# Kernel optimization log

Hardware: AMD Instinct MI355X
Metric: run time of the kernel (lower is better)

## Reference

```python
import jax, jax.numpy as jnp
import numpy as np
import itertools

DIM_X, DIM_Y = 3, 3
MAX_DIGIT = DIM_X * DIM_Y          # 9
NUM_NODES = MAX_DIGIT ** 2         # 81
EMBED = 16
HID = 96
BATCH = 256
ITERS = 4


def determine_edges(dim_x, dim_y):
    md = dim_x * dim_y
    rows = []
    for r in range(md):
        for c in range(md):
            s = {(r, i) for i in range(md)} | {(i, c) for i in range(md)}
            xm, ym = r // dim_x * dim_x, c // dim_y * dim_y
            s |= set(itertools.product(range(xm, xm + dim_x), range(ym, ym + dim_y)))
            s -= {(r, c)}
            rows.append(sorted(i * md + j for i, j in s))
    return np.asarray(rows, dtype=np.int32)  # [81, 20]


def mlp3(x, w0, b0, w1, b1, w2, b2):
    # MLP([a,b,c,d]): two ReLU hidden layers, linear output
    x = jax.nn.relu(x @ w0.T + b0)
    x = jax.nn.relu(x @ w1.T + b1)
    return x @ w2.T + b2


def setup_inputs() -> dict:
    key = jax.random.key(0)
    keys = iter(jax.random.split(key, 40))

    def lin(din, dout):
        kw, kb = jax.random.split(next(keys))
        lim = 1.0 / np.sqrt(din)
        w = jax.random.uniform(kw, (dout, din), jnp.float32, -lim, lim)
        b = jax.random.uniform(kb, (dout,), jnp.float32, -lim, lim)
        return w, b

    embed = jax.random.normal(next(keys), (MAX_DIGIT + 1, EMBED), jnp.float32)

    in_w0, in_b0 = lin(EMBED, HID); in_w1, in_b1 = lin(HID, HID); in_w2, in_b2 = lin(HID, HID)
    f_w0, f_b0 = lin(2 * HID, HID); f_w1, f_b1 = lin(HID, HID); f_w2, f_b2 = lin(HID, HID)
    g_w0, g_b0 = lin(2 * HID, HID); g_w1, g_b1 = lin(HID, HID); g_w2, g_b2 = lin(HID, HID)
    r_w0, r_b0 = lin(HID, HID); r_w1, r_b1 = lin(HID, HID); r_w2, r_b2 = lin(HID, MAX_DIGIT)

    lim = 1.0 / np.sqrt(HID)
    lstm_wih = jax.random.uniform(next(keys), (4 * HID, HID), jnp.float32, -lim, lim)
    lstm_whh = jax.random.uniform(next(keys), (4 * HID, HID), jnp.float32, -lim, lim)
    lstm_bih = jax.random.uniform(next(keys), (4 * HID,), jnp.float32, -lim, lim)
    lstm_bhh = jax.random.uniform(next(keys), (4 * HID,), jnp.float32, -lim, lim)

    grids = jax.random.randint(next(keys), (BATCH, NUM_NODES), 0, MAX_DIGIT + 1)
    c0 = jax.random.normal(next(keys), (BATCH * NUM_NODES, HID), jnp.float32)
    edges = jnp.asarray(determine_edges(DIM_X, DIM_Y))

    return dict(embed=embed,
                in_w0=in_w0, in_b0=in_b0, in_w1=in_w1, in_b1=in_b1, in_w2=in_w2, in_b2=in_b2,
                f_w0=f_w0, f_b0=f_b0, f_w1=f_w1, f_b1=f_b1, f_w2=f_w2, f_b2=f_b2,
                g_w0=g_w0, g_b0=g_b0, g_w1=g_w1, g_b1=g_b1, g_w2=g_w2, g_b2=g_b2,
                lstm_wih=lstm_wih, lstm_whh=lstm_whh, lstm_bih=lstm_bih, lstm_bhh=lstm_bhh,
                r_w0=r_w0, r_b0=r_b0, r_w1=r_w1, r_b1=r_b1, r_w2=r_w2, r_b2=r_b2,
                c0=c0, grids=grids, edges=edges, iters=ITERS)


def reference(embed,
              in_w0, in_b0, in_w1, in_b1, in_w2, in_b2,
              f_w0, f_b0, f_w1, f_b1, f_w2, f_b2,
              g_w0, g_b0, g_w1, g_b1, g_w2, g_b2,
              lstm_wih, lstm_whh, lstm_bih, lstm_bhh,
              r_w0, r_b0, r_w1, r_b1, r_w2, r_b2,
              c0, grids, edges, iters):
    B, N = grids.shape
    K = edges.shape[1]
    emb = embed[grids]                                   # [B, N, EMBED]
    X = mlp3(emb, in_w0, in_b0, in_w1, in_b1, in_w2, in_b2)  # [B, N, HID]
    H = X
    h = X.reshape(B * N, HID)
    c = c0
    outputs = []
    for _ in range(iters):
        # gather neighbor states: [B, N, K, HID]
        Hn = H[:, edges]
        Hs = jnp.broadcast_to(H[:, :, None, :], Hn.shape)
        pair = jnp.concatenate([Hs, Hn], axis=-1)        # [B, N, K, 2*HID]
        M = mlp3(pair, f_w0, f_b0, f_w1, f_b1, f_w2, f_b2).sum(axis=2)  # [B, N, HID]
        gin = mlp3(jnp.concatenate([X, M], axis=-1),
                   g_w0, g_b0, g_w1, g_b1, g_w2, g_b2).reshape(B * N, HID)
        # single-step LSTM (torch gate order: i, f, g, o)
        gates = gin @ lstm_wih.T + lstm_bih + h @ lstm_whh.T + lstm_bhh
        gi, gf, gg, go = jnp.split(gates, 4, axis=-1)
        c = jax.nn.sigmoid(gf) * c + jax.nn.sigmoid(gi) * jnp.tanh(gg)
        h = jax.nn.sigmoid(go) * jnp.tanh(c)
        H = h.reshape(B, N, HID)
        outputs.append(mlp3(H, r_w0, r_b0, r_w1, r_b1, r_w2, r_b2))  # [B, N, MAX_DIGIT]
    return jnp.stack(outputs)  # [iters, B, N, MAX_DIGIT]
```

## Files before the change

### kernel.cpp

```cpp
#include <hip/hip_runtime.h>
#include <hip/hip_bf16.h>

typedef __hip_bfloat16 bf16;
typedef __attribute__((ext_vector_type(8))) short short8;
typedef __attribute__((ext_vector_type(8))) __bf16 bf16x8;
typedef __attribute__((ext_vector_type(4))) float f32x4;

#define BN 20736
#define NNODE 81
#define KNB 20

__device__ inline float bf2f(short s) {
  union { unsigned u; float f; } x; x.u = ((unsigned)(unsigned short)s) << 16; return x.f;
}
__device__ inline short f2bf(float f) {
  __hip_bfloat16 h = __float2bfloat16(f);
  return *reinterpret_cast<short*>(&h);
}
__device__ inline bf16x8 ld8(const bf16* p) {
  return __builtin_bit_cast(bf16x8, *(const short8*)p);
}

__device__ inline void zacc3(f32x4 acc[3]) {
  #pragma unroll
  for (int nt = 0; nt < 3; ++nt) acc[nt] = (f32x4){0.f, 0.f, 0.f, 0.f};
}
__device__ inline void load_w48(const bf16* __restrict__ W, int ldw, int n0, int lr, int lq,
                                bf16x8 wf[3][3]) {
  #pragma unroll
  for (int nt = 0; nt < 3; ++nt)
    #pragma unroll
    for (int ks = 0; ks < 3; ++ks)
      wf[nt][ks] = ld8(&W[(size_t)(n0 + nt * 16 + lr) * ldw + ks * 32 + lq * 8]);
}
__device__ inline void gemm48(const bf16x8 af[3], const bf16x8 wf[3][3], f32x4 acc[3]) {
  #pragma unroll
  for (int ks = 0; ks < 3; ++ks)
    #pragma unroll
    for (int nt = 0; nt < 3; ++nt)
      acc[nt] = __builtin_amdgcn_mfma_f32_16x16x32_bf16(af[ks], wf[nt][ks], acc[nt], 0, 0, 0);
}
__device__ inline void acc_store_cs(float* xw, const f32x4 acc[3], int lr, int lq, int n0) {
  #pragma unroll
  for (int nt = 0; nt < 3; ++nt)
    #pragma unroll
    for (int r = 0; r < 4; ++r)
      xw[(lq * 4 + r) * 100 + n0 + nt * 16 + lr] = acc[nt][r];
}
__device__ inline void xbuf_frag(const float* xw, int lr, int lq,
                                 const float* __restrict__ bias, float bscale,
                                 const bf16* __restrict__ residRow, int act,
                                 bf16x8 af[3]) {
  #pragma unroll
  for (int ks = 0; ks < 3; ++ks) {
    const int c0 = ks * 32 + lq * 8;
    float4 x0 = *(const float4*)&xw[lr * 100 + c0];
    float4 x1 = *(const float4*)&xw[lr * 100 + c0 + 4];
    float xv[8] = {x0.x, x0.y, x0.z, x0.w, x1.x, x1.y, x1.z, x1.w};
    if (bias) {
      float4 b0 = *(const float4*)&bias[c0];
      float4 b1 = *(const float4*)&bias[c0 + 4];
      float bv[8] = {b0.x, b0.y, b0.z, b0.w, b1.x, b1.y, b1.z, b1.w};
      #pragma unroll
      for (int j = 0; j < 8; ++j) xv[j] += bscale * bv[j];
    }
    if (residRow) {
      short8 r8 = *(const short8*)&residRow[c0];
      #pragma unroll
      for (int j = 0; j < 8; ++j) xv[j] += bf2f(r8[j]);
    }
    short8 o;
    #pragma unroll
    for (int j = 0; j < 8; ++j) {
      float v = xv[j];
      if (act) v = fmaxf(v, 0.f);
      o[j] = f2bf(v);
    }
    af[ks] = __builtin_bit_cast(bf16x8, o);
  }
}
__device__ inline void store_frag(bf16* dst, int lq, const bf16x8 af[3]) {
  #pragma unroll
  for (int ks = 0; ks < 3; ++ks)
    *(short8*)&dst[ks * 32 + lq * 8] = __builtin_bit_cast(short8, af[ks]);
}

__global__ __launch_bounds__(256) void prep_k(
    const float* in_w1, const float* in_w2, const float* f_w1, const float* f_w2,
    const float* g_w1, const float* g_w2, const float* r_w0, const float* r_w1,
    const float* r_w2, const float* wih, const float* whh, const float* g_w0,
    const float* f_w0, const float* in_w0, const float* f_b0,
    bf16* inw1b, bf16* inw2b, bf16* fw1b, bf16* fw2b,
    bf16* gw1b, bf16* gw2b, bf16* rw0b, bf16* rw1b,
    bf16* rw2b, bf16* wihb, bf16* whhb, bf16* gw0b,
    bf16* wfnb, bf16* w0pb, float* bias_fn)
{
  int idx = blockIdx.x * 256 + threadIdx.x;
  int y = blockIdx.y;
  const float* src = nullptr; bf16* dst = nullptr; int cnt = 0;
  switch (y) {
    case 0:  src = in_w1; dst = inw1b; cnt = 9216;  break;
    case 1:  src = in_w2; dst = inw2b; cnt = 9216;  break;
    case 2:  src = f_w1;  dst = fw1b;  cnt = 9216;  break;
    case 3:  src = f_w2;  dst = fw2b;  cnt = 9216;  break;
    case 4:  src = g_w1;  dst = gw1b;  cnt = 9216;  break;
    case 5:  src = g_w2;  dst = gw2b;  cnt = 9216;  break;
    case 6:  src = r_w0;  dst = rw0b;  cnt = 9216;  break;
    case 7:  src = r_w1;  dst = rw1b;  cnt = 9216;  break;
    case 8:  src = r_w2;  dst = rw2b;  cnt = 864;   break;
    case 9:  src = wih;   dst = wihb;  cnt = 36864; break;
    case 10: src = whh;   dst = whhb;  cnt = 36864; break;
    case 11: src = g_w0;  dst = gw0b;  cnt = 18432; break;
    case 12: {
      if (idx < 18432) {
        int n = idx / 96, k = idx - n * 96;
        float v = (n < 96) ? f_w0[n * 192 + k] : f_w0[(n - 96) * 192 + 96 + k];
        wfnb[idx] = __float2bfloat16(v);
      }
      return;
    }
    case 13: {
      if (idx < 3072) {
        int n = idx >> 5, k = idx & 31;
        w0pb[idx] = __float2bfloat16(k < 16 ? in_w0[n * 16 + k] : 0.f);
      }
      return;
    }
    default: {
      if (idx < 192) bias_fn[idx] = (idx < 96) ? f_b0[idx] : 0.f;
      return;
    }
  }
  if (idx < cnt) dst[idx] = __float2bfloat16(src[idx]);
}

__global__ __launch_bounds__(256) void embed_k(const float* __restrict__ embed,
                                               const int* __restrict__ grids,
                                               bf16* __restrict__ emb) {
  int idx = blockIdx.x * 256 + threadIdx.x;
  if (idx >= BN * 32) return;
  int r = idx >> 5, k = idx & 31;
  emb[idx] = __float2bfloat16(k < 16 ? embed[grids[r] * 16 + k] : 0.f);
}

__global__ __launch_bounds__(256) void fused_in_k(
    const bf16* __restrict__ emb, const bf16* __restrict__ w0pb, const float* __restrict__ in_b0,
    const bf16* __restrict__ inw1b, const float* __restrict__ in_b1,
    const bf16* __restrict__ inw2b, const float* __restrict__ in_b2,
    const bf16* __restrict__ gw0b, const float* __restrict__ g_b0,
    const bf16* __restrict__ wfnb, const float* __restrict__ bias_fn,
    bf16* __restrict__ X, bf16* __restrict__ Xg, bf16* __restrict__ P)
{
  __shared__ float xbuf[2][2][1600];
  const int t = threadIdx.x, w = t >> 6, lane = t & 63, lr = lane & 15, lq = lane >> 4;
  const int mh = w >> 1, ch = w & 1, n0 = ch * 48;
  const int m0 = blockIdx.x * 32 + mh * 16;
  float* x0 = xbuf[0][mh];
  float* x1 = xbuf[1][mh];
  bf16x8 wf[3][3]; f32x4 acc[3]; bf16x8 af[3];

  bf16x8 a0 = ld8(&emb[(size_t)(m0 + lr) * 32 + lq * 8]);
  #pragma unroll
  for (int nt = 0; nt < 3; ++nt)
    wf[nt][0] = ld8(&w0pb[(size_t)(n0 + nt * 16 + lr) * 32 + lq * 8]);
  zacc3(acc);
  #pragma unroll
  for (int nt = 0; nt < 3; ++nt)
    acc[nt] = __builtin_amdgcn_mfma_f32_16x16x32_bf16(a0, wf[nt][0], acc[nt], 0, 0, 0);
  acc_store_cs(x0, acc, lr, lq, n0);
  __syncthreads();
  xbuf_frag(x0, lr, lq, in_b0, 1.f, nullptr, 1, af);
  load_w48(inw1b, 96, n0, lr, lq, wf); zacc3(acc); gemm48(af, wf, acc);
  acc_store_cs(x1, acc, lr, lq, n0);
  __syncthreads();
  xbuf_frag(x1, lr, lq, in_b1, 1.f, nullptr, 1, af);
  load_w48(inw2b, 96, n0, lr, lq, wf); zacc3(acc); gemm48(af, wf, acc);
  acc_store_cs(x0, acc, lr, lq, n0);
  __syncthreads();
  bf16x8 xf[3];
  xbuf_frag(x0, lr, lq, in_b2, 1.f, nullptr, 0, xf);
  if (ch == 0) store_frag(&X[(size_t)(m0 + lr) * 96], lq, xf);
  load_w48(gw0b, 192, n0, lr, lq, wf); zacc3(acc); gemm48(xf, wf, acc);
  acc_store_cs(x1, acc, lr, lq, n0);
  __syncthreads();
  xbuf_frag(x1, lr, lq, g_b0, 1.f, nullptr, 0, af);
  if (ch == 0) store_frag(&Xg[(size_t)(m0 + lr) * 96], lq, af);
  #pragma unroll
  for (int ph = 0; ph < 2; ++ph) {
    float* xb = ph ? x1 : x0;
    load_w48(wfnb + (size_t)ph * 96 * 96, 96, n0, lr, lq, wf); zacc3(acc); gemm48(xf, wf, acc);
    acc_store_cs(xb, acc, lr, lq, n0);
    __syncthreads();
    xbuf_frag(xb, lr, lq, bias_fn + ph * 96, 1.f, nullptr, 0, af);
    if (ch == 0) store_frag(&P[(size_t)(m0 + lr) * 192 + ph * 96], lq, af);
  }
}

__global__ __launch_bounds__(256) void edge_k(
    const bf16* __restrict__ P, const bf16* __restrict__ w1bf,
    const float* __restrict__ b1, const int* __restrict__ edges,
    const bf16* __restrict__ fw2b, const float* __restrict__ f_b2,
    bf16* __restrict__ M)
{
  __shared__ short zs[160 * 104];
  __shared__ short sbuf[16 * 104];
  const int t = threadIdx.x;
  const int ng0 = blockIdx.x * 2;
  for (int i = t; i < 8 * 104; i += 256) sbuf[(8 + i / 104) * 104 + (i % 104)] = 0;
  for (int cc = t; cc < 160 * 12; cc += 256) {
    int zrow = cc / 12, c8 = cc - zrow * 12;
    int g = zrow >= 80 ? 1 : 0;
    int row = zrow - g * 80;
    int p = row / 20, j = row - p * 20;
    int gr = (ng0 + g) * 4 + p;
    int b = gr / NNODE, i = gr - b * NNODE;
    int e = edges[i * KNB + j];
    short8 a8 = *(const short8*)&P[(size_t)gr * 192 + c8 * 8];
    short8 n8 = *(const short8*)&P[((size_t)b * NNODE + e) * 192 + 96 + c8 * 8];
    short8 z;
    #pragma unroll
    for (int q = 0; q < 8; ++q)
      z[q] = f2bf(fmaxf(bf2f(a8[q]) + bf2f(n8[q]), 0.f));
    *(short8*)&zs[zrow * 104 + c8 * 8] = z;
  }
  __syncthreads();

  const int w = t >> 6, lane = t & 63, lr = lane & 15, lq = lane >> 4;
  const int g = w >> 1, ch = w & 1, n0 = ch * 48, zb = g * 80;

  bf16x8 wf[3][3];
  #pragma unroll
  for (int nt = 0; nt < 3; ++nt)
    #pragma unroll
    for (int ks = 0; ks < 3; ++ks)
      wf[nt][ks] = ld8(&w1bf[(size_t)(n0 + nt * 16 + lr) * 96 + ks * 32 + lq * 8]);

  f32x4 acc[5][3];
  #pragma unroll
  for (int mt = 0; mt < 5; ++mt)
    #pragma unroll
    for (int nt = 0; nt < 3; ++nt) acc[mt][nt] = (f32x4){0.f, 0.f, 0.f, 0.f};

  #pragma unroll
  for (int ks = 0; ks < 3; ++ks) {
    const int koff = ks * 32 + lq * 8;
    #pragma unroll
    for (int mt = 0; mt < 5; ++mt) {
      bf16x8 af = __builtin_bit_cast(bf16x8, *(const short8*)&zs[(zb + mt * 16 + lr) * 104 + koff]);
      #pragma unroll
      for (int nt = 0; nt < 3; ++nt)
        acc[mt][nt] = __builtin_amdgcn_mfma_f32_16x16x32_bf16(af, wf[nt][ks], acc[mt][nt], 0, 0, 0);
    }
  }

  float bv[3];
  #pragma unroll
  for (int nt = 0; nt < 3; ++nt) bv[nt] = b1[n0 + nt * 16 + lr];
  float nodeacc[4][3];
  #pragma unroll
  for (int pp = 0; pp < 4; ++pp)
    #pragma unroll
    for (int nt = 0; nt < 3; ++nt) nodeacc[pp][nt] = 0.f;
  #pragma unroll
  for (int mt = 0; mt < 5; ++mt)
    #pragma unroll
    for (int nt = 0; nt < 3; ++nt)
      #pragma unroll
      for (int r = 0; r < 4; ++r) {
        int row = mt * 16 + lq * 4 + r;
        int p = row / 20;
        float v = fmaxf(acc[mt][nt][r] + bv[nt], 0.f);
        #pragma unroll
        for (int pp = 0; pp < 4; ++pp)
          nodeacc[pp][nt] += (p == pp) ? v : 0.f;
      }
  #pragma unroll
  for (int pp = 0; pp < 4; ++pp)
    #pragma unroll
    for (int nt = 0; nt < 3; ++nt) {
      float v = nodeacc[pp][nt];
      v += __shfl_xor(v, 16, 64);
      v += __shfl_xor(v, 32, 64);
      if (lq == 0)
        sbuf[(g * 4 + pp) * 104 + n0 + nt * 16 + lr] = f2bf(v);
    }
  __syncthreads();
  if (w < 2) {
    const int mn0 = w * 48;
    bf16x8 mwf[3][3];
    #pragma unroll
    for (int nt = 0; nt < 3; ++nt)
      #pragma unroll
      for (int ks = 0; ks < 3; ++ks)
        mwf[nt][ks] = ld8(&fw2b[(size_t)(mn0 + nt * 16 + lr) * 96 + ks * 32 + lq * 8]);
    f32x4 macc[3];
    zacc3(macc);
    #pragma unroll
    for (int ks = 0; ks < 3; ++ks) {
      bf16x8 af = __builtin_bit_cast(bf16x8, *(const short8*)&sbuf[lr * 104 + ks * 32 + lq * 8]);
      #pragma unroll
      for (int nt = 0; nt < 3; ++nt)
        macc[nt] = __builtin_amdgcn_mfma_f32_16x16x32_bf16(af, mwf[nt][ks], macc[nt], 0, 0, 0);
    }
    #pragma unroll
    for (int nt = 0; nt < 3; ++nt) {
      int col = mn0 + nt * 16 + lr;
      float bb = (float)KNB * f_b2[col];
      #pragma unroll
      for (int r = 0; r < 4; ++r) {
        int row = lq * 4 + r;
        if (row < 8)
          M[(size_t)(ng0 * 4 + row) * 96 + col] = __float2bfloat16(macc[nt][r] + bb);
      }
    }
  }
}

__global__ __launch_bounds__(256) void fused_iter_k(
    const bf16* __restrict__ Min,
    const bf16* __restrict__ gw0b, const bf16* __restrict__ Xg,
    const bf16* __restrict__ gw1b, const float* __restrict__ g_b1,
    const bf16* __restrict__ gw2b, const float* __restrict__ g_b2,
    const bf16* __restrict__ Hin,
    const bf16* __restrict__ wihb, const bf16* __restrict__ whhb,
    const float* __restrict__ bih, const float* __restrict__ bhh,
    float* __restrict__ c, bf16* __restrict__ Hout,
    const bf16* __restrict__ wfnb, const float* __restrict__ bias_fn, bf16* __restrict__ P,
    const bf16* __restrict__ rw0b, const float* __restrict__ r_b0,
    const bf16* __restrict__ rw1b, const float* __restrict__ r_b1,
    const bf16* __restrict__ rw2b, const float* __restrict__ r_b2,
    float* __restrict__ outp, int doP)
{
  __shared__ float xbuf[2][2][1600];
  const int t = threadIdx.x, w = t >> 6, lane = t & 63, lr = lane & 15, lq = lane >> 4;
  const int mh = w >> 1, ch = w & 1, n0 = ch * 48;
  const int m0 = blockIdx.x * 32 + mh * 16;
  float* x0 = xbuf[0][mh];
  float* x1 = xbuf[1][mh];
  bf16x8 wf[3][3]; f32x4 acc[3]; bf16x8 af[3];

  #pragma unroll
  for (int ks = 0; ks < 3; ++ks)
    af[ks] = ld8(&Min[(size_t)(m0 + lr) * 96 + ks * 32 + lq * 8]);
  load_w48(gw0b + 96, 192, n0, lr, lq, wf); zacc3(acc); gemm48(af, wf, acc);
  acc_store_cs(x0, acc, lr, lq, n0);
  __syncthreads();
  xbuf_frag(x0, lr, lq, nullptr, 0.f, &Xg[(size_t)(m0 + lr) * 96], 1, af);
  load_w48(gw1b, 96, n0, lr, lq, wf); zacc3(acc); gemm48(af, wf, acc);
  acc_store_cs(x1, acc, lr, lq, n0);
  __syncthreads();
  xbuf_frag(x1, lr, lq, g_b1, 1.f, nullptr, 1, af);
  load_w48(gw2b, 96, n0, lr, lq, wf); zacc3(acc); gemm48(af, wf, acc);
  acc_store_cs(x0, acc, lr, lq, n0);
  __syncthreads();
  bf16x8 gf[3];
  xbuf_frag(x0, lr, lq, g_b2, 1.f, nullptr, 0, gf);

  bf16x8 hin[3];
  #pragma unroll
  for (int ks = 0; ks < 3; ++ks)
    hin[ks] = ld8(&Hin[(size_t)(m0 + lr) * 96 + ks * 32 + lq * 8]);
  f32x4 ga[4][3];
  #pragma unroll
  for (int g4 = 0; g4 < 4; ++g4)
    #pragma unroll
    for (int nt = 0; nt < 3; ++nt) ga[g4][nt] = (f32x4){0.f, 0.f, 0.f, 0.f};
  #pragma unroll
  for (int g4 = 0; g4 < 4; ++g4)
    #pragma unroll
    for (int nt = 0; nt < 3; ++nt) {
      size_t nrow = (size_t)(g4 * 96 + n0 + nt * 16 + lr) * 96;
      #pragma unroll
      for (int ks = 0; ks < 3; ++ks) {
        ga[g4][nt] = __builtin_amdgcn_mfma_f32_16x16x32_bf16(
            gf[ks], ld8(&wihb[nrow + ks * 32 + lq * 8]), ga[g4][nt], 0, 0, 0);
        ga[g4][nt] = __builtin_amdgcn_mfma_f32_16x16x32_bf16(
            hin[ks], ld8(&whhb[nrow + ks * 32 + lq * 8]), ga[g4][nt], 0, 0, 0);
      }
    }
  #pragma unroll
  for (int nt = 0; nt < 3; ++nt) {
    int col = n0 + nt * 16 + lr;
    float bvi = bih[col] + bhh[col];
    float bvf = bih[96 + col] + bhh[96 + col];
    float bvg = bih[192 + col] + bhh[192 + col];
    float bvo = bih[288 + col] + bhh[288 + col];
    #pragma unroll
    for (int r = 0; r < 4; ++r) {
      int m = m0 + lq * 4 + r;
      size_t idx = (size_t)m * 96 + col;
      float gi = ga[0][nt][r] + bvi;
      float gfv = ga[1][nt][r] + bvf;
      float gg = ga[2][nt][r] + bvg;
      float go = ga[3][nt][r] + bvo;
      float si = 1.f / (1.f + expf(-gi));
      float sf = 1.f / (1.f + expf(-gfv));
      float so = 1.f / (1.f + expf(-go));
      float tg = tanhf(gg);
      float cn = sf * c[idx] + si * tg;
      c[idx] = cn;
      float ho = so * tanhf(cn);
      Hout[idx] = __float2bfloat16(ho);
      x1[(lq * 4 + r) * 100 + col] = ho;
    }
  }
  __syncthreads();
  bf16x8 hf[3];
  xbuf_frag(x1, lr, lq, nullptr, 0.f, nullptr, 0, hf);

  if (doP) {
    #pragma unroll
    for (int ph = 0; ph < 2; ++ph) {
      float* xb = ph ? x1 : x0;
      load_w48(wfnb + (size_t)ph * 96 * 96, 96, n0, lr, lq, wf); zacc3(acc); gemm48(hf, wf, acc);
      acc_store_cs(xb, acc, lr, lq, n0);
      __syncthreads();
      xbuf_frag(xb, lr, lq, bias_fn + ph * 96, 1.f, nullptr, 0, af);
      if (ch == 0) store_frag(&P[(size_t)(m0 + lr) * 192 + ph * 96], lq, af);
    }
  }

  load_w48(rw0b, 96, n0, lr, lq, wf); zacc3(acc); gemm48(hf, wf, acc);
  acc_store_cs(x0, acc, lr, lq, n0);
  __syncthreads();
  xbuf_frag(x0, lr, lq, r_b0, 1.f, nullptr, 1, af);
  load_w48(rw1b, 96, n0, lr, lq, wf); zacc3(acc); gemm48(af, wf, acc);
  acc_store_cs(x1, acc, lr, lq, n0);
  __syncthreads();
  xbuf_frag(x1, lr, lq, r_b1, 1.f, nullptr, 1, af);
  if (ch == 0) {
    bf16x8 w9[3];
    #pragma unroll
    for (int ks = 0; ks < 3; ++ks) {
      short8 s = {0, 0, 0, 0, 0, 0, 0, 0};
      if (lr < 9) s = *(const short8*)&rw2b[(size_t)lr * 96 + ks * 32 + lq * 8];
      w9[ks] = __builtin_bit_cast(bf16x8, s);
    }
    f32x4 a9 = (f32x4){0.f, 0.f, 0.f, 0.f};
    #pragma unroll
    for (int ks = 0; ks < 3; ++ks)
      a9 = __builtin_amdgcn_mfma_f32_16x16x32_bf16(af[ks], w9[ks], a9, 0, 0, 0);
    if (lr < 9) {
      float bb = r_b2[lr];
      #pragma unroll
      for (int r = 0; r < 4; ++r)
        outp[(size_t)(m0 + lq * 4 + r) * 9 + lr] = a9[r] + bb;
    }
  }
}

extern "C" void kernel_launch(void* const* d_in, const int* in_sizes, int n_in,
                              void* d_out, int out_size, void* d_ws, size_t ws_size,
                              hipStream_t stream) {
  const float* embed   = (const float*)d_in[0];
  const float* in_w0   = (const float*)d_in[1];
  const float* in_b0   = (const float*)d_in[2];
  const float* in_w1   = (const float*)d_in[3];
  const float* in_b1   = (const float*)d_in[4];
  const float* in_w2   = (const float*)d_in[5];
  const float* in_b2   = (const float*)d_in[6];
  const float* f_w0    = (const float*)d_in[7];
  const float* f_b0    = (const float*)d_in[8];
  const float* f_w1    = (const float*)d_in[9];
  const float* f_b1    = (const float*)d_in[10];
  const float* f_w2    = (const float*)d_in[11];
  const float* f_b2    = (const float*)d_in[12];
  const float* g_w0    = (const float*)d_in[13];
  const float* g_b0    = (const float*)d_in[14];
  const float* g_w1    = (const float*)d_in[15];
  const float* g_b1    = (const float*)d_in[16];
  const float* g_w2    = (const float*)d_in[17];
  const float* g_b2    = (const float*)d_in[18];
  const float* wih     = (const float*)d_in[19];
  const float* whh     = (const float*)d_in[20];
  const float* bih     = (const float*)d_in[21];
  const float* bhh     = (const float*)d_in[22];
  const float* r_w0    = (const float*)d_in[23];
  const float* r_b0    = (const float*)d_in[24];
  const float* r_w1    = (const float*)d_in[25];
  const float* r_b1    = (const float*)d_in[26];
  const float* r_w2    = (const float*)d_in[27];
  const float* r_b2    = (const float*)d_in[28];
  const float* c0      = (const float*)d_in[29];
  const int*   grids   = (const int*)d_in[30];
  const int*   edges   = (const int*)d_in[31];

  float* out = (float*)d_out;
  const int iters = out_size / (BN * 9);

  float* c    = (float*)d_ws;
  bf16* H0    = (bf16*)(c + (size_t)BN * 96);
  bf16* H1    = H0 + (size_t)BN * 96;
  bf16* Xg    = H1 + (size_t)BN * 96;
  bf16* P     = Xg + (size_t)BN * 96;
  bf16* Mb    = P  + (size_t)BN * 192;
  bf16* emb   = Mb + (size_t)BN * 96;
  bf16* w0pb  = emb + (size_t)BN * 32;
  bf16* wfnb  = w0pb + 3072;
  bf16* inw1b = wfnb + 18432;
  bf16* inw2b = inw1b + 9216;
  bf16* fw1b  = inw2b + 9216;
  bf16* fw2b  = fw1b + 9216;
  bf16* gw0b  = fw2b + 9216;
  bf16* gw1b  = gw0b + 18432;
  bf16* gw2b  = gw1b + 9216;
  bf16* rw0b  = gw2b + 9216;
  bf16* rw1b  = rw0b + 9216;
  bf16* rw2b  = rw1b + 9216;
  bf16* wihb  = rw2b + 864;
  bf16* whhb  = wihb + 36864;
  float* bias_fn = (float*)(whhb + 36864);

  prep_k<<<dim3(144, 15), 256, 0, stream>>>(
      in_w1, in_w2, f_w1, f_w2, g_w1, g_w2, r_w0, r_w1, r_w2, wih, whh, g_w0,
      f_w0, in_w0, f_b0,
      inw1b, inw2b, fw1b, fw2b, gw1b, gw2b, rw0b, rw1b, rw2b, wihb, whhb, gw0b,
      wfnb, w0pb, bias_fn);
  embed_k<<<(BN * 32) / 256, 256, 0, stream>>>(embed, grids, emb);
  fused_in_k<<<BN / 32, 256, 0, stream>>>(emb, w0pb, in_b0, inw1b, in_b1, inw2b, in_b2,
                                          gw0b, g_b0, wfnb, bias_fn, H0, Xg, P);
  hipMemcpyAsync(c, c0, (size_t)BN * 96 * sizeof(float), hipMemcpyDeviceToDevice, stream);

  for (int it = 0; it < iters; ++it) {
    bf16* Hin  = (it & 1) ? H1 : H0;
    bf16* Hout = (it & 1) ? H0 : H1;
    edge_k<<<BN / 8, 256, 0, stream>>>(P, fw1b, f_b1, edges, fw2b, f_b2, Mb);
    fused_iter_k<<<BN / 32, 256, 0, stream>>>(
        Mb, gw0b, Xg, gw1b, g_b1, gw2b, g_b2,
        Hin, wihb, whhb, bih, bhh, c, Hout,
        wfnb, bias_fn, P, rw0b, r_b0, rw1b, r_b1, rw2b, r_b2,
        out + (size_t)it * BN * 9, it < iters - 1 ? 1 : 0);
  }
}
```

Measured before the change: 336.5 us.

## Repartition fused iteration kernel to 16-row tiles across six column waves

Restructures fused_iter_k so each 384-thread block handles 16 rows, with six waves each owning 16 output columns instead of 2x2 waves owning 48 columns. Input rows (M, X, H) are staged into shared memory and outputs (H, P) are written with coalesced 16-byte stores from shared buffers. On the last iteration the c and H writes are skipped because nothing reads them afterward. edge_k block indices are also swizzled to change the order in which the gather touches P. The price is more blocks and barriers, plus repeated weight-fragment loads per 16-row tile.

Result: slower. 345.9 us (+2.8%).

```diff
diff --git a/kernel.cpp b/kernel.cpp
--- a/kernel.cpp
+++ b/kernel.cpp
@@ -47,9 +47,20 @@
     for (int r = 0; r < 4; ++r)
       xw[(lq * 4 + r) * 100 + n0 + nt * 16 + lr] = acc[nt][r];
 }
+__device__ inline void load_w16(const bf16* __restrict__ W, int ldw, int n0, int lr, int lq,
+                                bf16x8 wf[3]) {
+  #pragma unroll
+  for (int ks = 0; ks < 3; ++ks)
+    wf[ks] = ld8(&W[(size_t)(n0 + lr) * ldw + ks * 32 + lq * 8]);
+}
+__device__ inline void gemm16(const bf16x8 af[3], const bf16x8 wf[3], f32x4& acc) {
+  #pragma unroll
+  for (int ks = 0; ks < 3; ++ks)
+    acc = __builtin_amdgcn_mfma_f32_16x16x32_bf16(af[ks], wf[ks], acc, 0, 0, 0);
+}
 __device__ inline void xbuf_frag(const float* xw, int lr, int lq,
                                  const float* __restrict__ bias, float bscale,
-                                 const bf16* __restrict__ residRow, int act,
+                                 const bf16* residRow, int act,
                                  bf16x8 af[3]) {
   #pragma unroll
   for (int ks = 0; ks < 3; ++ks) {
@@ -205,7 +216,8 @@
   __shared__ short zs[160 * 104];
   __shared__ short sbuf[16 * 104];
   const int t = threadIdx.x;
-  const int ng0 = blockIdx.x * 2;
+  const int swz = (blockIdx.x & 7) * 324 + (blockIdx.x >> 3);
+  const int ng0 = swz * 2;
   for (int i = t; i < 8 * 104; i += 256) sbuf[(8 + i / 104) * 104 + (i % 104)] = 0;
   for (int cc = t; cc < 160 * 12; cc += 256) {
     int zrow = cc / 12, c8 = cc - zrow * 12;
@@ -316,7 +328,7 @@
   }
 }
 
-__global__ __launch_bounds__(256) void fused_iter_k(
+__global__ __launch_bounds__(384) void fused_iter_k(
     const bf16* __restrict__ Min,
     const bf16* __restrict__ gw0b, const bf16* __restrict__ Xg,
     const bf16* __restrict__ gw1b, const float* __restrict__ g_b1,
@@ -331,56 +343,65 @@
     const bf16* __restrict__ rw2b, const float* __restrict__ r_b2,
     float* __restrict__ outp, int doP)
 {
-  __shared__ float xbuf[2][2][1600];
+  __shared__ short ab[3][16 * 104];
+  __shared__ float xb0[1600], xb1[1600];
   const int t = threadIdx.x, w = t >> 6, lane = t & 63, lr = lane & 15, lq = lane >> 4;
-  const int mh = w >> 1, ch = w & 1, n0 = ch * 48;
-  const int m0 = blockIdx.x * 32 + mh * 16;
-  float* x0 = xbuf[0][mh];
-  float* x1 = xbuf[1][mh];
-  bf16x8 wf[3][3]; f32x4 acc[3]; bf16x8 af[3];
+  const int n0 = w * 16;
+  const int m0 = blockIdx.x * 16;
+
+  for (int cc = t; cc < 576; cc += 384) {
+    int arr = cc / 192, rem = cc - arr * 192, row = rem / 12, c8 = rem - row * 12;
+    const bf16* src = arr == 0 ? Min : (arr == 1 ? Xg : Hin);
+    *(short8*)&ab[arr][row * 104 + c8 * 8] =
+        *(const short8*)&src[(size_t)(m0 + row) * 96 + c8 * 8];
+  }
+  __syncthreads();
+
+  bf16x8 wf[3], af[3];
+  f32x4 acc;
 
   #pragma unroll
   for (int ks = 0; ks < 3; ++ks)
-    af[ks] = ld8(&Min[(size_t)(m0 + lr) * 96 + ks * 32 + lq * 8]);
-  load_w48(gw0b + 96, 192, n0, lr, lq, wf); zacc3(acc); gemm48(af, wf, acc);
-  acc_store_cs(x0, acc, lr, lq, n0);
-  __syncthreads();
-  xbuf_frag(x0, lr, lq, nullptr, 0.f, &Xg[(size_t)(m0 + lr) * 96], 1, af);
-  load_w48(gw1b, 96, n0, lr, lq, wf); zacc3(acc); gemm48(af, wf, acc);
-  acc_store_cs(x1, acc, lr, lq, n0);
-  __syncthreads();
-  xbuf_frag(x1, lr, lq, g_b1, 1.f, nullptr, 1, af);
-  load_w48(gw2b, 96, n0, lr, lq, wf); zacc3(acc); gemm48(af, wf, acc);
-  acc_store_cs(x0, acc, lr, lq, n0);
-  __syncthreads();
-  bf16x8 gf[3];
-  xbuf_frag(x0, lr, lq, g_b2, 1.f, nullptr, 0, gf);
-
-  bf16x8 hin[3];
+    af[ks] = ld8((const bf16*)&ab[0][lr * 104 + ks * 32 + lq * 8]);
+  load_w16(gw0b + 96, 192, n0, lr, lq, wf);
+  acc = (f32x4){0.f, 0.f, 0.f, 0.f}; gemm16(af, wf, acc);
+  #pragma unroll
+  for (int r = 0; r < 4; ++r) xb0[(lq * 4 + r) * 100 + n0 + lr] = acc[r];
+  __syncthreads();
+  xbuf_frag(xb0, lr, lq, nullptr, 0.f, (const bf16*)&ab[1][lr * 104], 1, af);
+  load_w16(gw1b, 96, n0, lr, lq, wf);
+  acc = (f32x4){0.f, 0.f, 0.f, 0.f}; gemm16(af, wf, acc);
+  #pragma unroll
+  for (int r = 0; r < 4; ++r) xb1[(lq * 4 + r) * 100 + n0 + lr] = acc[r];
+  __syncthreads();
+  xbuf_frag(xb1, lr, lq, g_b1, 1.f, nullptr, 1, af);
+  load_w16(gw2b, 96, n0, lr, lq, wf);
+  acc = (f32x4){0.f, 0.f, 0.f, 0.f}; gemm16(af, wf, acc);
+  #pragma unroll
+  for (int r = 0; r < 4; ++r) xb0[(lq * 4 + r) * 100 + n0 + lr] = acc[r];
+  __syncthreads();
+
+  bf16x8 gf[3], hin[3];
+  xbuf_frag(xb0, lr, lq, g_b2, 1.f, nullptr, 0, gf);
   #pragma unroll
   for (int ks = 0; ks < 3; ++ks)
-    hin[ks] = ld8(&Hin[(size_t)(m0 + lr) * 96 + ks * 32 + lq * 8]);
-  f32x4 ga[4][3];
-  #pragma unroll
-  for (int g4 = 0; g4 < 4; ++g4)
-    #pragma unroll
-    for (int nt = 0; nt < 3; ++nt) ga[g4][nt] = (f32x4){0.f, 0.f, 0.f, 0.f};
-  #pragma unroll
-  for (int g4 = 0; g4 < 4; ++g4)
-    #pragma unroll
-    for (int nt = 0; nt < 3; ++nt) {
-      size_t nrow = (size_t)(g4 * 96 + n0 + nt * 16 + lr) * 96;
-      #pragma unroll
-      for (int ks = 0; ks < 3; ++ks) {
-        ga[g4][nt] = __builtin_amdgcn_mfma_f32_16x16x32_bf16(
-            gf[ks], ld8(&wihb[nrow + ks * 32 + lq * 8]), ga[g4][nt], 0, 0, 0);
-        ga[g4][nt] = __builtin_amdgcn_mfma_f32_16x16x32_bf16(
-            hin[ks], ld8(&whhb[nrow + ks * 32 + lq * 8]), ga[g4][nt], 0, 0, 0);
-      }
-    }
-  #pragma unroll
-  for (int nt = 0; nt < 3; ++nt) {
-    int col = n0 + nt * 16 + lr;
+    hin[ks] = ld8((const bf16*)&ab[2][lr * 104 + ks * 32 + lq * 8]);
+  f32x4 ga[4];
+  #pragma unroll
+  for (int g4 = 0; g4 < 4; ++g4) ga[g4] = (f32x4){0.f, 0.f, 0.f, 0.f};
+  #pragma unroll
+  for (int g4 = 0; g4 < 4; ++g4) {
+    size_t nrow = (size_t)(g4 * 96 + n0 + lr) * 96;
+    #pragma unroll
+    for (int ks = 0; ks < 3; ++ks) {
+      ga[g4] = __builtin_amdgcn_mfma_f32_16x16x32_bf16(
+          gf[ks], ld8(&wihb[nrow + ks * 32 + lq * 8]), ga[g4], 0, 0, 0);
+      ga[g4] = __builtin_amdgcn_mfma_f32_16x16x32_bf16(
+          hin[ks], ld8(&whhb[nrow + ks * 32 + lq * 8]), ga[g4], 0, 0, 0);
+    }
+  }
+  {
+    const int col = n0 + lr;
     float bvi = bih[col] + bhh[col];
     float bvf = bih[96 + col] + bhh[96 + col];
     float bvg = bih[192 + col] + bhh[192 + col];
@@ -389,46 +410,79 @@
     for (int r = 0; r < 4; ++r) {
       int m = m0 + lq * 4 + r;
       size_t idx = (size_t)m * 96 + col;
-      float gi = ga[0][nt][r] + bvi;
-      float gfv = ga[1][nt][r] + bvf;
-      float gg = ga[2][nt][r] + bvg;
-      float go = ga[3][nt][r] + bvo;
+      float gi = ga[0][r] + bvi;
+      float gfv = ga[1][r] + bvf;
+      float gg = ga[2][r] + bvg;
+      float go = ga[3][r] + bvo;
       float si = 1.f / (1.f + expf(-gi));
       float sf = 1.f / (1.f + expf(-gfv));
       float so = 1.f / (1.f + expf(-go));
       float tg = tanhf(gg);
       float cn = sf * c[idx] + si * tg;
-      c[idx] = cn;
-      float ho = so * tanhf(cn);
-      Hout[idx] = __float2bfloat16(ho);
-      x1[(lq * 4 + r) * 100 + col] = ho;
-    }
-  }
-  __syncthreads();
+      if (doP) c[idx] = cn;
+      xb1[(lq * 4 + r) * 100 + col] = so * tanhf(cn);
+    }
+  }
+  __syncthreads();
+
   bf16x8 hf[3];
-  xbuf_frag(x1, lr, lq, nullptr, 0.f, nullptr, 0, hf);
+  xbuf_frag(xb1, lr, lq, nullptr, 0.f, nullptr, 0, hf);
 
   if (doP) {
-    #pragma unroll
-    for (int ph = 0; ph < 2; ++ph) {
-      float* xb = ph ? x1 : x0;
-      load_w48(wfnb + (size_t)ph * 96 * 96, 96, n0, lr, lq, wf); zacc3(acc); gemm48(hf, wf, acc);
-      acc_store_cs(xb, acc, lr, lq, n0);
-      __syncthreads();
-      xbuf_frag(xb, lr, lq, bias_fn + ph * 96, 1.f, nullptr, 0, af);
-      if (ch == 0) store_frag(&P[(size_t)(m0 + lr) * 192 + ph * 96], lq, af);
-    }
-  }
-
-  load_w48(rw0b, 96, n0, lr, lq, wf); zacc3(acc); gemm48(hf, wf, acc);
-  acc_store_cs(x0, acc, lr, lq, n0);
-  __syncthreads();
-  xbuf_frag(x0, lr, lq, r_b0, 1.f, nullptr, 1, af);
-  load_w48(rw1b, 96, n0, lr, lq, wf); zacc3(acc); gemm48(af, wf, acc);
-  acc_store_cs(x1, acc, lr, lq, n0);
-  __syncthreads();
-  xbuf_frag(x1, lr, lq, r_b1, 1.f, nullptr, 1, af);
-  if (ch == 0) {
+    if (t < 192) {
+      int row = t / 12, c8 = t - row * 12;
+      short8 o;
+      #pragma unroll
+      for (int j = 0; j < 8; ++j) o[j] = f2bf(xb1[row * 100 + c8 * 8 + j]);
+      *(short8*)&Hout[(size_t)(m0 + row) * 96 + c8 * 8] = o;
+    }
+    load_w16(wfnb, 96, n0, lr, lq, wf);
+    acc = (f32x4){0.f, 0.f, 0.f, 0.f}; gemm16(hf, wf, acc);
+    {
+      float bv = bias_fn[n0 + lr];
+      #pragma unroll
+      for (int r = 0; r < 4; ++r) xb0[(lq * 4 + r) * 100 + n0 + lr] = acc[r] + bv;
+    }
+    __syncthreads();
+    if (t < 192) {
+      int row = t / 12, c8 = t - row * 12;
+      short8 o;
+      #pragma unroll
+      for (int j = 0; j < 8; ++j) o[j] = f2bf(xb0[row * 100 + c8 * 8 + j]);
+      *(short8*)&P[(size_t)(m0 + row) * 192 + c8 * 8] = o;
+    }
+    load_w16(wfnb + 96 * 96, 96, n0, lr, lq, wf);
+    acc = (f32x4){0.f, 0.f, 0.f, 0.f}; gemm16(hf, wf, acc);
+    {
+      float bv = bias_fn[96 + n0 + lr];
+      #pragma unroll
+      for (int r = 0; r < 4; ++r) xb1[(lq * 4 + r) * 100 + n0 + lr] = acc[r] + bv;
+    }
+    __syncthreads();
+    if (t < 192) {
+      int row = t / 12, c8 = t - row * 12;
+      short8 o;
+      #pragma unroll
+      for (int j = 0; j < 8; ++j) o[j] = f2bf(xb1[row * 100 + c8 * 8 + j]);
+      *(short8*)&P[(size_t)(m0 + row) * 192 + 96 + c8 * 8] = o;
+    }
+  }
+
+  load_w16(rw0b, 96, n0, lr, lq, wf);
+  acc = (f32x4){0.f, 0.f, 0.f, 0.f}; gemm16(hf, wf, acc);
+  __syncthreads();
+  #pragma unroll
+  for (int r = 0; r < 4; ++r) xb0[(lq * 4 + r) * 100 + n0 + lr] = acc[r];
+  __syncthreads();
+  xbuf_frag(xb0, lr, lq, r_b0, 1.f, nullptr, 1, af);
+  load_w16(rw1b, 96, n0, lr, lq, wf);
+  acc = (f32x4){0.f, 0.f, 0.f, 0.f}; gemm16(af, wf, acc);
+  __syncthreads();
+  #pragma unroll
+  for (int r = 0; r < 4; ++r) xb1[(lq * 4 + r) * 100 + n0 + lr] = acc[r];
+  __syncthreads();
+  xbuf_frag(xb1, lr, lq, r_b1, 1.f, nullptr, 1, af);
+  if (w == 0) {
     bf16x8 w9[3];
     #pragma unroll
     for (int ks = 0; ks < 3; ++ks) {
@@ -525,7 +579,7 @@
     bf16* Hin  = (it & 1) ? H1 : H0;
     bf16* Hout = (it & 1) ? H0 : H1;
     edge_k<<<BN / 8, 256, 0, stream>>>(P, fw1b, f_b1, edges, fw2b, f_b2, Mb);
-    fused_iter_k<<<BN / 32, 256, 0, stream>>>(
+    fused_iter_k<<<BN / 16, 384, 0, stream>>>(
         Mb, gw0b, Xg, gw1b, g_b1, gw2b, g_b2,
         Hin, wihb, whhb, bih, bhh, c, Hout,
         wfnb, bias_fn, P, rw0b, r_b0, rw1b, r_b1, rw2b, r_b2,
```

## Restructure iteration kernel into 16-row blocks with double-buffered weight prefetch

Applied to the files above, without the earlier changes.

The fused iteration kernel moves to 128-thread blocks covering 16 rows each, with two waves splitting the 96 output columns. Weights for the next GEMM are prefetched into a second register set while the current GEMM runs. The cell state is loaded early, and on the last iteration the c and H writes are skipped; H and P are now written with cooperative vectorised stores from shared memory. The edge kernel gets a swizzled block order and hoists its weight loads above the gather, at the cost of more register pressure from the doubled weight fragments.

New measurement: 331.6 us. About the same (-1.5%).

```diff
diff --git a/kernel.cpp b/kernel.cpp
--- a/kernel.cpp
+++ b/kernel.cpp
@@ -49,7 +49,7 @@
 }
 __device__ inline void xbuf_frag(const float* xw, int lr, int lq,
                                  const float* __restrict__ bias, float bscale,
-                                 const bf16* __restrict__ residRow, int act,
+                                 const bf16* residRow, int act,
                                  bf16x8 af[3]) {
   #pragma unroll
   for (int ks = 0; ks < 3; ++ks) {
@@ -205,14 +205,25 @@
   __shared__ short zs[160 * 104];
   __shared__ short sbuf[16 * 104];
   const int t = threadIdx.x;
-  const int ng0 = blockIdx.x * 2;
+  const int swz = (blockIdx.x & 7) * 324 + (blockIdx.x >> 3);
+  const int ng0 = swz * 2;
+  const int w = t >> 6, lane = t & 63, lr = lane & 15, lq = lane >> 4;
+  const int g = w >> 1, ch = w & 1, n0 = ch * 48, zb = g * 80;
+
+  bf16x8 wf[3][3];
+  #pragma unroll
+  for (int nt = 0; nt < 3; ++nt)
+    #pragma unroll
+    for (int ks = 0; ks < 3; ++ks)
+      wf[nt][ks] = ld8(&w1bf[(size_t)(n0 + nt * 16 + lr) * 96 + ks * 32 + lq * 8]);
+
   for (int i = t; i < 8 * 104; i += 256) sbuf[(8 + i / 104) * 104 + (i % 104)] = 0;
   for (int cc = t; cc < 160 * 12; cc += 256) {
     int zrow = cc / 12, c8 = cc - zrow * 12;
-    int g = zrow >= 80 ? 1 : 0;
-    int row = zrow - g * 80;
+    int gg = zrow >= 80 ? 1 : 0;
+    int row = zrow - gg * 80;
     int p = row / 20, j = row - p * 20;
-    int gr = (ng0 + g) * 4 + p;
+    int gr = (ng0 + gg) * 4 + p;
     int b = gr / NNODE, i = gr - b * NNODE;
     int e = edges[i * KNB + j];
     short8 a8 = *(const short8*)&P[(size_t)gr * 192 + c8 * 8];
@@ -224,16 +235,6 @@
     *(short8*)&zs[zrow * 104 + c8 * 8] = z;
   }
   __syncthreads();
-
-  const int w = t >> 6, lane = t & 63, lr = lane & 15, lq = lane >> 4;
-  const int g = w >> 1, ch = w & 1, n0 = ch * 48, zb = g * 80;
-
-  bf16x8 wf[3][3];
-  #pragma unroll
-  for (int nt = 0; nt < 3; ++nt)
-    #pragma unroll
-    for (int ks = 0; ks < 3; ++ks)
-      wf[nt][ks] = ld8(&w1bf[(size_t)(n0 + nt * 16 + lr) * 96 + ks * 32 + lq * 8]);
 
   f32x4 acc[5][3];
   #pragma unroll
@@ -316,7 +317,7 @@
   }
 }
 
-__global__ __launch_bounds__(256) void fused_iter_k(
+__global__ __launch_bounds__(128) void fused_iter_k(
     const bf16* __restrict__ Min,
     const bf16* __restrict__ gw0b, const bf16* __restrict__ Xg,
     const bf16* __restrict__ gw1b, const float* __restrict__ g_b1,
@@ -331,35 +332,46 @@
     const bf16* __restrict__ rw2b, const float* __restrict__ r_b2,
     float* __restrict__ outp, int doP)
 {
-  __shared__ float xbuf[2][2][1600];
+  __shared__ float xb0[1600], xb1[1600];
   const int t = threadIdx.x, w = t >> 6, lane = t & 63, lr = lane & 15, lq = lane >> 4;
-  const int mh = w >> 1, ch = w & 1, n0 = ch * 48;
-  const int m0 = blockIdx.x * 32 + mh * 16;
-  float* x0 = xbuf[0][mh];
-  float* x1 = xbuf[1][mh];
-  bf16x8 wf[3][3]; f32x4 acc[3]; bf16x8 af[3];
+  const int n0 = w * 48;
+  const int m0 = blockIdx.x * 16;
+
+  bf16x8 wfA[3][3], wfB[3][3], af[3];
+  f32x4 acc[3];
 
   #pragma unroll
   for (int ks = 0; ks < 3; ++ks)
     af[ks] = ld8(&Min[(size_t)(m0 + lr) * 96 + ks * 32 + lq * 8]);
-  load_w48(gw0b + 96, 192, n0, lr, lq, wf); zacc3(acc); gemm48(af, wf, acc);
-  acc_store_cs(x0, acc, lr, lq, n0);
-  __syncthreads();
-  xbuf_frag(x0, lr, lq, nullptr, 0.f, &Xg[(size_t)(m0 + lr) * 96], 1, af);
-  load_w48(gw1b, 96, n0, lr, lq, wf); zacc3(acc); gemm48(af, wf, acc);
-  acc_store_cs(x1, acc, lr, lq, n0);
-  __syncthreads();
-  xbuf_frag(x1, lr, lq, g_b1, 1.f, nullptr, 1, af);
-  load_w48(gw2b, 96, n0, lr, lq, wf); zacc3(acc); gemm48(af, wf, acc);
-  acc_store_cs(x0, acc, lr, lq, n0);
-  __syncthreads();
-  bf16x8 gf[3];
-  xbuf_frag(x0, lr, lq, g_b2, 1.f, nullptr, 0, gf);
-
   bf16x8 hin[3];
   #pragma unroll
   for (int ks = 0; ks < 3; ++ks)
     hin[ks] = ld8(&Hin[(size_t)(m0 + lr) * 96 + ks * 32 + lq * 8]);
+
+  load_w48(gw0b + 96, 192, n0, lr, lq, wfA);
+  zacc3(acc); gemm48(af, wfA, acc);
+  load_w48(gw1b, 96, n0, lr, lq, wfB);
+  acc_store_cs(xb0, acc, lr, lq, n0);
+  __syncthreads();
+  xbuf_frag(xb0, lr, lq, nullptr, 0.f, &Xg[(size_t)(m0 + lr) * 96], 1, af);
+  zacc3(acc); gemm48(af, wfB, acc);
+  load_w48(gw2b, 96, n0, lr, lq, wfA);
+  acc_store_cs(xb1, acc, lr, lq, n0);
+  __syncthreads();
+  xbuf_frag(xb1, lr, lq, g_b1, 1.f, nullptr, 1, af);
+  zacc3(acc); gemm48(af, wfA, acc);
+  acc_store_cs(xb0, acc, lr, lq, n0);
+  __syncthreads();
+  bf16x8 gf[3];
+  xbuf_frag(xb0, lr, lq, g_b2, 1.f, nullptr, 0, gf);
+
+  float cv[3][4];
+  #pragma unroll
+  for (int nt = 0; nt < 3; ++nt)
+    #pragma unroll
+    for (int r = 0; r < 4; ++r)
+      cv[nt][r] = c[(size_t)(m0 + lq * 4 + r) * 96 + n0 + nt * 16 + lr];
+
   f32x4 ga[4][3];
   #pragma unroll
   for (int g4 = 0; g4 < 4; ++g4)
@@ -397,38 +409,71 @@
       float sf = 1.f / (1.f + expf(-gfv));
       float so = 1.f / (1.f + expf(-go));
       float tg = tanhf(gg);
-      float cn = sf * c[idx] + si * tg;
-      c[idx] = cn;
-      float ho = so * tanhf(cn);
-      Hout[idx] = __float2bfloat16(ho);
-      x1[(lq * 4 + r) * 100 + col] = ho;
+      float cn = sf * cv[nt][r] + si * tg;
+      if (doP) c[idx] = cn;
+      xb1[(lq * 4 + r) * 100 + col] = so * tanhf(cn);
     }
   }
   __syncthreads();
   bf16x8 hf[3];
-  xbuf_frag(x1, lr, lq, nullptr, 0.f, nullptr, 0, hf);
+  xbuf_frag(xb1, lr, lq, nullptr, 0.f, nullptr, 0, hf);
 
   if (doP) {
-    #pragma unroll
-    for (int ph = 0; ph < 2; ++ph) {
-      float* xb = ph ? x1 : x0;
-      load_w48(wfnb + (size_t)ph * 96 * 96, 96, n0, lr, lq, wf); zacc3(acc); gemm48(hf, wf, acc);
-      acc_store_cs(xb, acc, lr, lq, n0);
-      __syncthreads();
-      xbuf_frag(xb, lr, lq, bias_fn + ph * 96, 1.f, nullptr, 0, af);
-      if (ch == 0) store_frag(&P[(size_t)(m0 + lr) * 192 + ph * 96], lq, af);
-    }
-  }
-
-  load_w48(rw0b, 96, n0, lr, lq, wf); zacc3(acc); gemm48(hf, wf, acc);
-  acc_store_cs(x0, acc, lr, lq, n0);
-  __syncthreads();
-  xbuf_frag(x0, lr, lq, r_b0, 1.f, nullptr, 1, af);
-  load_w48(rw1b, 96, n0, lr, lq, wf); zacc3(acc); gemm48(af, wf, acc);
-  acc_store_cs(x1, acc, lr, lq, n0);
-  __syncthreads();
-  xbuf_frag(x1, lr, lq, r_b1, 1.f, nullptr, 1, af);
-  if (ch == 0) {
+    for (int cc = t; cc < 192; cc += 128) {
+      int row = cc / 12, c8 = cc - row * 12;
+      short8 o;
+      #pragma unroll
+      for (int j = 0; j < 8; ++j) o[j] = f2bf(xb1[row * 100 + c8 * 8 + j]);
+      *(short8*)&Hout[(size_t)(m0 + row) * 96 + c8 * 8] = o;
+    }
+    load_w48(wfnb, 96, n0, lr, lq, wfA);
+    zacc3(acc); gemm48(hf, wfA, acc);
+    load_w48(wfnb + 96 * 96, 96, n0, lr, lq, wfB);
+    #pragma unroll
+    for (int nt = 0; nt < 3; ++nt) {
+      float bvv = bias_fn[n0 + nt * 16 + lr];
+      #pragma unroll
+      for (int r = 0; r < 4; ++r)
+        xb0[(lq * 4 + r) * 100 + n0 + nt * 16 + lr] = acc[nt][r] + bvv;
+    }
+    __syncthreads();
+    for (int cc = t; cc < 192; cc += 128) {
+      int row = cc / 12, c8 = cc - row * 12;
+      short8 o;
+      #pragma unroll
+      for (int j = 0; j < 8; ++j) o[j] = f2bf(xb0[row * 100 + c8 * 8 + j]);
+      *(short8*)&P[(size_t)(m0 + row) * 192 + c8 * 8] = o;
+    }
+    zacc3(acc); gemm48(hf, wfB, acc);
+    #pragma unroll
+    for (int nt = 0; nt < 3; ++nt) {
+      float bvv = bias_fn[96 + n0 + nt * 16 + lr];
+      #pragma unroll
+      for (int r = 0; r < 4; ++r)
+        xb1[(lq * 4 + r) * 100 + n0 + nt * 16 + lr] = acc[nt][r] + bvv;
+    }
+    __syncthreads();
+    for (int cc = t; cc < 192; cc += 128) {
+      int row = cc / 12, c8 = cc - row * 12;
+      short8 o;
+      #pragma unroll
+      for (int j = 0; j < 8; ++j) o[j] = f2bf(xb1[row * 100 + c8 * 8 + j]);
+      *(short8*)&P[(size_t)(m0 + row) * 192 + 96 + c8 * 8] = o;
+    }
+  }
+
+  load_w48(rw0b, 96, n0, lr, lq, wfA);
+  zacc3(acc); gemm48(hf, wfA, acc);
+  load_w48(rw1b, 96, n0, lr, lq, wfB);
+  __syncthreads();
+  acc_store_cs(xb0, acc, lr, lq, n0);
+  __syncthreads();
+  xbuf_frag(xb0, lr, lq, r_b0, 1.f, nullptr, 1, af);
+  zacc3(acc); gemm48(af, wfB, acc);
+  acc_store_cs(xb1, acc, lr, lq, n0);
+  __syncthreads();
+  xbuf_frag(xb1, lr, lq, r_b1, 1.f, nullptr, 1, af);
+  if (w == 0) {
     bf16x8 w9[3];
     #pragma unroll
     for (int ks = 0; ks < 3; ++ks) {
@@ -525,7 +570,7 @@
     bf16* Hin  = (it & 1) ? H1 : H0;
     bf16* Hout = (it & 1) ? H0 : H1;
     edge_k<<<BN / 8, 256, 0, stream>>>(P, fw1b, f_b1, edges, fw2b, f_b2, Mb);
-    fused_iter_k<<<BN / 32, 256, 0, stream>>>(
+    fused_iter_k<<<BN / 16, 128, 0, stream>>>(
         Mb, gw0b, Xg, gw1b, g_b1, gw2b, g_b2,
         Hin, wihb, whhb, bih, bhh, c, Hout,
         wfnb, bias_fn, P, rw0b, r_b0, rw1b, r_b1, rw2b, r_b2,
```
